# Performance work log

Measured on AMD Instinct MI355X. Metric: run time of the kernel, lower is better.

The kernel has to match this reference:

```python
import jax, jax.numpy as jnp
import numpy as np

B, NP, NS, CIN, COUT, CMID = 16, 1024, 32, 64, 128, 32

def _bn(x, g, b, m, v, eps=1e-5):
    # inference-mode BatchNorm over channel axis 1
    sh = (1, -1) + (1,) * (x.ndim - 2)
    return (x - m.reshape(sh)) * (g.reshape(sh) * jax.lax.rsqrt(v.reshape(sh) + eps)) + b.reshape(sh)

def setup_inputs() -> dict:
    key = jax.random.key(0)
    ks = jax.random.split(key, 10)
    f = jax.random.normal
    return {
        "new_xyz": f(ks[0], (B, 3, NP), jnp.float32),
        "grouped_xyz": f(ks[1], (B, NP, NS, 3), jnp.float32),
        "grouped_feature": f(ks[2], (B, CIN, NS, NP), jnp.float32),
        "wh_w": f(ks[3], (CMID, 3), jnp.float32) * 0.1,
        "wh_b": f(ks[4], (CMID,), jnp.float32) * 0.1,
        "wh_g": jnp.ones((CMID,), jnp.float32), "wh_beta": jnp.zeros((CMID,), jnp.float32),
        "wh_m": jnp.zeros((CMID,), jnp.float32), "wh_v": jnp.ones((CMID,), jnp.float32),
        "n1_w": f(ks[5], (16, 1), jnp.float32) * 0.1,
        "n1_b": f(ks[6], (16,), jnp.float32) * 0.1,
        "n1_g": jnp.ones((16,), jnp.float32), "n1_beta": jnp.zeros((16,), jnp.float32),
        "n1_m": jnp.zeros((16,), jnp.float32), "n1_v": jnp.ones((16,), jnp.float32),
        "n2_w": f(ks[7], (1, 16), jnp.float32) * 0.1,
        "n2_b": f(ks[8], (1,), jnp.float32) * 0.1,
        "n2_g": jnp.ones((1,), jnp.float32), "n2_beta": jnp.zeros((1,), jnp.float32),
        "n2_m": jnp.zeros((1,), jnp.float32), "n2_v": jnp.ones((1,), jnp.float32),
        "out_w": f(ks[9], (COUT, CIN, CMID), jnp.float32) * 0.05,
        "out_b": jnp.zeros((COUT,), jnp.float32),
        "out_g": jnp.ones((COUT,), jnp.float32), "out_beta": jnp.zeros((COUT,), jnp.float32),
        "out_m": jnp.zeros((COUT,), jnp.float32), "out_v": jnp.ones((COUT,), jnp.float32),
    }

def reference(new_xyz, grouped_xyz, grouped_feature,
              wh_w, wh_b, wh_g, wh_beta, wh_m, wh_v,
              n1_w, n1_b, n1_g, n1_beta, n1_m, n1_v,
              n2_w, n2_b, n2_g, n2_beta, n2_m, n2_v,
              out_w, out_b, out_g, out_beta, out_m, out_v):
    # kernel_density_estimation_ball mutates in place: after i=0 the reference
    # point is zero, so ONLY sample 0 is actually zeroed. Replicate exactly.
    gx = grouped_xyz.at[:, :, 0, :].set(0.0)          # [B,NP,NS,3]
    density = jnp.sum(gx, axis=-1, keepdims=True)      # [B,NP,NS,1]
    density = jnp.where(density < 1e-10, 1e-10, density)
    inv = 1.0 / density
    ds = inv / jnp.max(inv, axis=2, keepdims=True)     # [B,NP,NS,1]
    # weight net on the mutated grouped_xyz
    gx_p = jnp.transpose(gx, (0, 3, 1, 2))             # [B,3,NP,NS]
    w = jax.nn.relu(_bn(jnp.einsum('bcps,oc->bops', gx_p, wh_w) + wh_b.reshape(1, -1, 1, 1),
                        wh_g, wh_beta, wh_m, wh_v))    # [B,CMID,NP,NS]
    # nonlinear density transform
    dsp = jnp.transpose(ds, (0, 3, 1, 2))              # [B,1,NP,NS]
    d1 = jax.nn.relu(_bn(jnp.einsum('bcps,oc->bops', dsp, n1_w) + n1_b.reshape(1, -1, 1, 1),
                         n1_g, n1_beta, n1_m, n1_v))   # [B,16,NP,NS]
    d2 = jax.nn.sigmoid(_bn(jnp.einsum('bcps,oc->bops', d1, n2_w) + n2_b.reshape(1, -1, 1, 1),
                            n2_g, n2_beta, n2_m, n2_v))  # [B,1,NP,NS]
    # density-scaled features, then batched matmul with positional weights
    gf = jnp.transpose(grouped_feature, (0, 1, 3, 2)) * d2      # [B,CIN,NP,NS]
    mm = jnp.einsum('bcps,bmps->bcpm', gf, w)                   # [B,CIN,NP,CMID]
    # out_conv: Conv2d(CIN->COUT, kernel (1,CMID)) collapses last dim
    out = jnp.einsum('bcpk,ock->bop', mm, out_w) + out_b.reshape(1, -1, 1)  # [B,COUT,NP]
    out = _bn(out, out_g, out_beta, out_m, out_v)
    return (jnp.transpose(new_xyz, (0, 2, 1)), out)
```

## Files before the change

### kernel.cpp

```cpp
#include <hip/hip_runtime.h>
#include <hip/hip_bf16.h>


#define NPP 1024
#define NSS 32

typedef __attribute__((ext_vector_type(8))) short short8;
typedef __attribute__((ext_vector_type(4))) float f32x4;

__device__ __forceinline__ unsigned short f2bf(float x) {
  union { float f; unsigned u; } v; v.f = x;
  unsigned r = v.u + 0x7FFFu + ((v.u >> 16) & 1u);
  return (unsigned short)(r >> 16);
}

__device__ __forceinline__ unsigned long long pack4bf(f32x4 v) {
  return (unsigned long long)f2bf(v[0])
       | ((unsigned long long)f2bf(v[1]) << 16)
       | ((unsigned long long)f2bf(v[2]) << 32)
       | ((unsigned long long)f2bf(v[3]) << 48);
}

__global__ __launch_bounds__(256) void k_prep(
    const float* __restrict__ out_w, const float* __restrict__ new_xyz,
    unsigned short* __restrict__ owc, float* __restrict__ out0)
{
  int bid = blockIdx.x, t = threadIdx.x;
  if (bid < 128) {
    int gid = bid * 256 + t;
    int lane = gid & 63, ci = gid >> 6;
    int hi = ci & 1, tt = (ci >> 1) & 15, cblk = (ci >> 5) & 3, w = ci >> 7;
    int sg = lane >> 4, l15 = lane & 15;
    int o = w*32 + hi*16 + l15;
    int k = tt*2 + (sg >> 1);
    int cbase = cblk*16 + (sg & 1)*8;
    short8 vv;
    #pragma unroll
    for (int j = 0; j < 8; ++j)
      vv[j] = (short)f2bf(out_w[(o*64 + cbase + j)*32 + k]);
    *(short8*)&owc[(size_t)gid * 8] = vv;
  } else {
    int idx = (bid - 128) * 256 + t;
    int b = idx / 3072, r = idx - b*3072, p = r / 3, d = r - p*3;
    out0[idx] = new_xyz[(b*3 + d)*NPP + p];
  }
}

__global__ __launch_bounds__(256) void k_xpose(
    const float* __restrict__ F, unsigned short* __restrict__ Fb)
{
  int bid = blockIdx.x;
  int xcd = bid & 7, idx = bid >> 3;
  int b = xcd * 2 + (idx >> 4), ptq = idx & 15;
  int t = threadIdx.x;
  int sg = t >> 6, l15 = (t >> 2) & 15, k4 = t & 3;

  #pragma unroll
  for (int cblk = 0; cblk < 4; ++cblk) {
    int c = cblk * 16 + l15;
    const float* src = &F[((size_t)((b*64 + c)*32) + sg*8)*NPP + ptq*64 + k4*4];
    #pragma unroll
    for (int ptl = 0; ptl < 4; ++ptl) {
      float4 v[8];
      #pragma unroll
      for (int j = 0; j < 8; ++j) v[j] = *(const float4*)&src[(size_t)j*NPP + ptl*16];
      unsigned short* tb = &Fb[(size_t)(b*64 + ptq*4 + ptl)*32768 + cblk*512 + sg*128 + l15*8];
      #pragma unroll
      for (int pwl = 0; pwl < 4; ++pwl) {
        unsigned o0 = (unsigned)f2bf(((const float*)&v[0])[pwl]) | ((unsigned)f2bf(((const float*)&v[1])[pwl]) << 16);
        unsigned o1 = (unsigned)f2bf(((const float*)&v[2])[pwl]) | ((unsigned)f2bf(((const float*)&v[3])[pwl]) << 16);
        unsigned o2 = (unsigned)f2bf(((const float*)&v[4])[pwl]) | ((unsigned)f2bf(((const float*)&v[5])[pwl]) << 16);
        unsigned o3 = (unsigned)f2bf(((const float*)&v[6])[pwl]) | ((unsigned)f2bf(((const float*)&v[7])[pwl]) << 16);
        uint4 wv = {o0, o1, o2, o3};
        *(uint4*)&tb[(size_t)(k4*4 + pwl)*2048] = wv;
      }
    }
  }
}

struct Smem2 {
  float gxd[64*32*4];
  unsigned short wd[16*32*32];
  char mm[64*1024];
  float cst[192];
};

__global__ __launch_bounds__(512, 1) void k_main(
    const unsigned short* __restrict__ Fb, const float* __restrict__ GX,
    const float* __restrict__ whw, const float* __restrict__ whb,
    const float* __restrict__ whg, const float* __restrict__ whbeta,
    const float* __restrict__ whm, const float* __restrict__ whv,
    const float* __restrict__ n1w, const float* __restrict__ n1b,
    const float* __restrict__ n1g, const float* __restrict__ n1beta,
    const float* __restrict__ n1m, const float* __restrict__ n1v,
    const float* __restrict__ n2w, const float* __restrict__ n2b,
    const float* __restrict__ n2g, const float* __restrict__ n2beta,
    const float* __restrict__ n2m, const float* __restrict__ n2v,
    const unsigned short* __restrict__ OWc,
    const float* __restrict__ ob, const float* __restrict__ og,
    const float* __restrict__ obeta, const float* __restrict__ om,
    const float* __restrict__ ov,
    float* __restrict__ out1)
{
  __shared__ Smem2 sm;
  int xcd = blockIdx.x & 7, idx = blockIdx.x >> 3;
  int b = xcd*2 + (idx >> 4), pt64 = idx & 15;
  int p0 = pt64 * 64;
  int t = threadIdx.x, w = t >> 6, lane = t & 63;
  int l15 = lane & 15, sg = lane >> 4;

  int pp8 = t >> 3, si8 = t & 7;
  const float* g = &GX[(size_t)(b*NPP + p0 + pp8)*96 + si8*12];
  float4 f0 = *(const float4*)g;
  float4 f1 = *(const float4*)(g + 4);
  float4 f2 = *(const float4*)(g + 8);

  if (t < 32) {
    float sc = whg[t] * rsqrtf(whv[t] + 1e-5f);
    sm.cst[t]    = whw[t*3+0] * sc;
    sm.cst[32+t] = whw[t*3+1] * sc;
    sm.cst[64+t] = whw[t*3+2] * sc;
    sm.cst[96+t] = (whb[t] - whm[t]) * sc + whbeta[t];
  } else if (t < 48) {
    int i = t - 32;
    float sc = n1g[i] * rsqrtf(n1v[i] + 1e-5f);
    sm.cst[128+i] = n1w[i] * sc;
    sm.cst[144+i] = (n1b[i] - n1m[i]) * sc + n1beta[i];
  } else if (t < 64) {
    int i = t - 48;
    float sc = n2g[0] * rsqrtf(n2v[0] + 1e-5f);
    sm.cst[160+i] = n2w[i] * sc;
    if (i == 0) sm.cst[176] = (n2b[0] - n2m[0]) * sc + n2beta[0];
  }
  __syncthreads();

  {
    float xs[4], ys[4], zs[4], inv[4];
    xs[0]=f0.x; ys[0]=f0.y; zs[0]=f0.z;
    xs[1]=f0.w; ys[1]=f1.x; zs[1]=f1.y;
    xs[2]=f1.z; ys[2]=f1.w; zs[2]=f2.x;
    xs[3]=f2.y; ys[3]=f2.z; zs[3]=f2.w;
    if (si8 == 0) { xs[0]=0.f; ys[0]=0.f; zs[0]=0.f; }
    float mx = 0.f;
    #pragma unroll
    for (int u = 0; u < 4; ++u) {
      float den = xs[u] + ys[u] + zs[u];
      if (den < 1e-10f) den = 1e-10f;
      inv[u] = 1.0f / den;
      mx = fmaxf(mx, inv[u]);
    }
    #pragma unroll
    for (int m = 1; m < 8; m <<= 1) mx = fmaxf(mx, __shfl_xor(mx, m, 8));
    #pragma unroll
    for (int u = 0; u < 4; ++u) {
      float ds = inv[u] / mx;
      float acc = sm.cst[176];
      #pragma unroll
      for (int i = 0; i < 16; ++i) {
        float d1 = fmaxf(ds * sm.cst[128+i] + sm.cst[144+i], 0.f);
        acc += d1 * sm.cst[160+i];
      }
      float d2 = 1.0f / (1.0f + expf(-acc));
      float4 st = {xs[u], ys[u], zs[u], d2};
      *(float4*)&sm.gxd[(size_t)(pp8*32 + si8*4 + u)*4] = st;
    }
  }
  __syncthreads();

  const f32x4 z4 = {0,0,0,0};
  int phKh = (lane >> 4) & 1;
  int phPp = w*2 + (lane >> 5);
  int phSi = lane & 15;
  int ppA = w*2, ppB = w*2 + 1;
  int c0 = l15*32 + sg*8;

  short8 afA[4][4], afB[4][4];
  short8 bfrA[4][2], bfrB[4][2];
  #pragma unroll
  for (int pg = 0; pg < 4; ++pg) {
    const unsigned short* ft = &Fb[(size_t)(b*64 + pt64*4 + pg)*32768 + sg*128 + l15*8];
    #pragma unroll
    for (int cblk = 0; cblk < 4; ++cblk) {
      afA[pg][cblk] = *(const short8*)&ft[(size_t)ppA*2048 + cblk*512];
      afB[pg][cblk] = *(const short8*)&ft[(size_t)ppB*2048 + cblk*512];
    }
    const float4 ga = *(const float4*)&sm.gxd[(size_t)((pg*16 + phPp)*32 + phSi*2)*4];
    const float4 gb = *(const float4*)&sm.gxd[(size_t)((pg*16 + phPp)*32 + phSi*2 + 1)*4];
    #pragma unroll
    for (int ki = 0; ki < 16; ++ki) {
      int k = phKh*16 + ki;
      float a0 = sm.cst[k], a1 = sm.cst[32+k], a2 = sm.cst[64+k], bc = sm.cst[96+k];
      float w0 = fmaxf(ga.x*a0 + ga.y*a1 + ga.z*a2 + bc, 0.f) * ga.w;
      float w1 = fmaxf(gb.x*a0 + gb.y*a1 + gb.z*a2 + bc, 0.f) * gb.w;
      unsigned r = (unsigned)f2bf(w0) | ((unsigned)f2bf(w1) << 16);
      *(unsigned*)&sm.wd[(phPp*32 + k)*32 + phSi*2] = r;
    }
    #pragma unroll
    for (int kh = 0; kh < 2; ++kh) {
      bfrA[pg][kh] = *(const short8*)&sm.wd[(ppA*32 + kh*16 + l15)*32 + sg*8];
      bfrB[pg][kh] = *(const short8*)&sm.wd[(ppB*32 + kh*16 + l15)*32 + sg*8];
    }
  }

  int w4 = w & 3, gp0 = (w >> 2) * 2;
  f32x4 acc00 = {0,0,0,0}, acc10 = {0,0,0,0}, acc01 = {0,0,0,0}, acc11 = {0,0,0,0};
  int rowG0 = gp0*16 + l15, rowG1 = (gp0+1)*16 + l15;
  unsigned sw0 = (rowG0 & 15) << 4, sw1 = (rowG1 & 15) << 4;
  const char* bbase0 = sm.mm + rowG0*1024;
  const char* bbase1 = sm.mm + rowG1*1024;

  #pragma unroll
  for (int cblk = 0; cblk < 4; ++cblk) {
    #pragma unroll
    for (int pg = 0; pg < 4; ++pg) {
      f32x4 mA0 = __builtin_amdgcn_mfma_f32_16x16x32_bf16(afA[pg][cblk], bfrA[pg][0], z4, 0,0,0);
      f32x4 mA1 = __builtin_amdgcn_mfma_f32_16x16x32_bf16(afA[pg][cblk], bfrA[pg][1], z4, 0,0,0);
      f32x4 mB0 = __builtin_amdgcn_mfma_f32_16x16x32_bf16(afB[pg][cblk], bfrB[pg][0], z4, 0,0,0);
      f32x4 mB1 = __builtin_amdgcn_mfma_f32_16x16x32_bf16(afB[pg][cblk], bfrB[pg][1], z4, 0,0,0);
      int rowA = pg*16 + ppA, rowB = pg*16 + ppB;
      unsigned swA = (rowA & 15) << 4, swB = (rowB & 15) << 4;
      char* bA = sm.mm + rowA*1024;
      char* bB = sm.mm + rowB*1024;
      *(unsigned long long*)(bA + ((c0      ) ^ swA)) = pack4bf(mA0);
      *(unsigned long long*)(bA + ((c0 + 512) ^ swA)) = pack4bf(mA1);
      *(unsigned long long*)(bB + ((c0      ) ^ swB)) = pack4bf(mB0);
      *(unsigned long long*)(bB + ((c0 + 512) ^ swB)) = pack4bf(mB1);
    }
    __syncthreads();
    {
      const unsigned short* ac = &OWc[(size_t)((w4*4 + cblk)*16)*1024 + lane*8];
      #pragma unroll 8
      for (int tt = 0; tt < 16; ++tt) {
        short8 a0 = *(const short8*)&ac[tt*1024];
        short8 a1 = *(const short8*)&ac[tt*1024 + 512];
        int col = sg*16 + tt*64;
        short8 b0 = *(const short8*)(bbase0 + (col ^ sw0));
        short8 b1 = *(const short8*)(bbase1 + (col ^ sw1));
        acc00 = __builtin_amdgcn_mfma_f32_16x16x32_bf16(a0, b0, acc00, 0,0,0);
        acc10 = __builtin_amdgcn_mfma_f32_16x16x32_bf16(a1, b0, acc10, 0,0,0);
        acc01 = __builtin_amdgcn_mfma_f32_16x16x32_bf16(a0, b1, acc01, 0,0,0);
        acc11 = __builtin_amdgcn_mfma_f32_16x16x32_bf16(a1, b1, acc11, 0,0,0);
      }
    }
    __syncthreads();
  }

  #pragma unroll
  for (int hi = 0; hi < 2; ++hi)
    #pragma unroll
    for (int gg = 0; gg < 2; ++gg) {
      f32x4 a = hi ? (gg ? acc11 : acc10) : (gg ? acc01 : acc00);
      #pragma unroll
      for (int r = 0; r < 4; ++r) {
        int o = w4*32 + hi*16 + sg*4 + r;
        float sc = og[o] * rsqrtf(ov[o] + 1e-5f);
        float dd = (ob[o] - om[o]) * sc + obeta[o];
        out1[(size_t)(b*128 + o)*NPP + p0 + (gp0+gg)*16 + l15] = a[r] * sc + dd;
      }
    }
}

extern "C" void kernel_launch(void* const* d_in, const int* in_sizes, int n_in,
                              void* d_out, int out_size, void* d_ws, size_t ws_size,
                              hipStream_t stream) {
  (void)in_sizes; (void)n_in; (void)out_size; (void)ws_size;
  const float* new_xyz = (const float*)d_in[0];
  const float* gxyz    = (const float*)d_in[1];
  const float* gfeat   = (const float*)d_in[2];
  const float* whw     = (const float*)d_in[3];
  const float* whb     = (const float*)d_in[4];
  const float* whg     = (const float*)d_in[5];
  const float* whbeta  = (const float*)d_in[6];
  const float* whm     = (const float*)d_in[7];
  const float* whv     = (const float*)d_in[8];
  const float* n1w     = (const float*)d_in[9];
  const float* n1b     = (const float*)d_in[10];
  const float* n1g     = (const float*)d_in[11];
  const float* n1beta  = (const float*)d_in[12];
  const float* n1m     = (const float*)d_in[13];
  const float* n1v     = (const float*)d_in[14];
  const float* n2w     = (const float*)d_in[15];
  const float* n2b     = (const float*)d_in[16];
  const float* n2g     = (const float*)d_in[17];
  const float* n2beta  = (const float*)d_in[18];
  const float* n2m     = (const float*)d_in[19];
  const float* n2v     = (const float*)d_in[20];
  const float* out_w   = (const float*)d_in[21];
  const float* out_b   = (const float*)d_in[22];
  const float* out_g   = (const float*)d_in[23];
  const float* out_bt  = (const float*)d_in[24];
  const float* out_m   = (const float*)d_in[25];
  const float* out_v   = (const float*)d_in[26];

  unsigned short* owc = (unsigned short*)d_ws;
  unsigned short* fb  = owc + (1u << 18);
  float* out0 = (float*)d_out;
  float* out1 = out0 + 16*1024*3;

  hipLaunchKernelGGL(k_prep,  dim3(320), dim3(256), 0, stream, out_w, new_xyz, owc, out0);
  hipLaunchKernelGGL(k_xpose, dim3(256), dim3(256), 0, stream, gfeat, fb);
  hipLaunchKernelGGL(k_main,  dim3(256), dim3(512), 0, stream,
      fb, gxyz, whw, whb, whg, whbeta, whm, whv,
      n1w, n1b, n1g, n1beta, n1m, n1v,
      n2w, n2b, n2g, n2beta, n2m, n2v,
      owc, out_b, out_g, out_bt, out_m, out_v, out1);
}
```

Baseline: 87.02 us.

## Fuse feature transpose into main kernel with LDS staging and prefetch

Removes the separate k_xpose kernel, which converted grouped_feature to bf16 in a transposed layout in global memory. k_main now loads fp32 features directly, converts them and writes them into a swizzled LDS buffer that is unioned with the phase-0 scratch. It prefetches the next channel block's features into registers while the current block's MFMAs run. This saves a kernel launch and a full bf16 write and read round trip through global memory, at the cost of extra syncthreads, LDS traffic and register pressure in k_main.

```diff
diff --git a/kernel.cpp b/kernel.cpp
--- a/kernel.cpp
+++ b/kernel.cpp
@@ -3,7 +3,6 @@
 
 
 #define NPP 1024
-#define NSS 32
 
 typedef __attribute__((ext_vector_type(8))) short short8;
 typedef __attribute__((ext_vector_type(4))) float f32x4;
@@ -46,47 +45,20 @@
   }
 }
 
-__global__ __launch_bounds__(256) void k_xpose(
-    const float* __restrict__ F, unsigned short* __restrict__ Fb)
-{
-  int bid = blockIdx.x;
-  int xcd = bid & 7, idx = bid >> 3;
-  int b = xcd * 2 + (idx >> 4), ptq = idx & 15;
-  int t = threadIdx.x;
-  int sg = t >> 6, l15 = (t >> 2) & 15, k4 = t & 3;
-
-  #pragma unroll
-  for (int cblk = 0; cblk < 4; ++cblk) {
-    int c = cblk * 16 + l15;
-    const float* src = &F[((size_t)((b*64 + c)*32) + sg*8)*NPP + ptq*64 + k4*4];
-    #pragma unroll
-    for (int ptl = 0; ptl < 4; ++ptl) {
-      float4 v[8];
-      #pragma unroll
-      for (int j = 0; j < 8; ++j) v[j] = *(const float4*)&src[(size_t)j*NPP + ptl*16];
-      unsigned short* tb = &Fb[(size_t)(b*64 + ptq*4 + ptl)*32768 + cblk*512 + sg*128 + l15*8];
-      #pragma unroll
-      for (int pwl = 0; pwl < 4; ++pwl) {
-        unsigned o0 = (unsigned)f2bf(((const float*)&v[0])[pwl]) | ((unsigned)f2bf(((const float*)&v[1])[pwl]) << 16);
-        unsigned o1 = (unsigned)f2bf(((const float*)&v[2])[pwl]) | ((unsigned)f2bf(((const float*)&v[3])[pwl]) << 16);
-        unsigned o2 = (unsigned)f2bf(((const float*)&v[4])[pwl]) | ((unsigned)f2bf(((const float*)&v[5])[pwl]) << 16);
-        unsigned o3 = (unsigned)f2bf(((const float*)&v[6])[pwl]) | ((unsigned)f2bf(((const float*)&v[7])[pwl]) << 16);
-        uint4 wv = {o0, o1, o2, o3};
-        *(uint4*)&tb[(size_t)(k4*4 + pwl)*2048] = wv;
-      }
-    }
-  }
-}
-
-struct Smem2 {
-  float gxd[64*32*4];
-  unsigned short wd[16*32*32];
+struct Smem3 {
+  union {
+    struct {
+      float gxd[64*32*4];
+      unsigned short wd[16*32*32];
+    } ph0;
+    unsigned short fs[32768];
+  } u;
   char mm[64*1024];
   float cst[192];
 };
 
 __global__ __launch_bounds__(512, 1) void k_main(
-    const unsigned short* __restrict__ Fb, const float* __restrict__ GX,
+    const float* __restrict__ F, const float* __restrict__ GX,
     const float* __restrict__ whw, const float* __restrict__ whb,
     const float* __restrict__ whg, const float* __restrict__ whbeta,
     const float* __restrict__ whm, const float* __restrict__ whv,
@@ -102,12 +74,24 @@
     const float* __restrict__ ov,
     float* __restrict__ out1)
 {
-  __shared__ Smem2 sm;
+  __shared__ Smem3 sm;
   int xcd = blockIdx.x & 7, idx = blockIdx.x >> 3;
   int b = xcd*2 + (idx >> 4), pt64 = idx & 15;
   int p0 = pt64 * 64;
   int t = threadIdx.x, w = t >> 6, lane = t & 63;
   int l15 = lane & 15, sg = lane >> 4;
+
+  int so = w & 3, ch = w >> 2;
+  int q4 = lane & 3, c3 = (lane >> 2) & 7, jh = (lane >> 5) & 1;
+  int c_l = ch*8 + c3, s0 = so*8 + jh*4;
+  const float* fsrc0 = &F[((size_t)((b*64 + c_l)*32) + s0)*NPP + p0 + q4*4];
+
+  float4 fv[4][4];
+  #pragma unroll
+  for (int jj = 0; jj < 4; ++jj)
+    #pragma unroll
+    for (int qg = 0; qg < 4; ++qg)
+      fv[jj][qg] = *(const float4*)&fsrc0[(size_t)jj*NPP + qg*16];
 
   int pp8 = t >> 3, si8 = t & 7;
   const float* g = &GX[(size_t)(b*NPP + p0 + pp8)*96 + si8*12];
@@ -162,7 +146,7 @@
       }
       float d2 = 1.0f / (1.0f + expf(-acc));
       float4 st = {xs[u], ys[u], zs[u], d2};
-      *(float4*)&sm.gxd[(size_t)(pp8*32 + si8*4 + u)*4] = st;
+      *(float4*)&sm.u.ph0.gxd[(size_t)(pp8*32 + si8*4 + u)*4] = st;
     }
   }
   __syncthreads();
@@ -174,18 +158,11 @@
   int ppA = w*2, ppB = w*2 + 1;
   int c0 = l15*32 + sg*8;
 
-  short8 afA[4][4], afB[4][4];
   short8 bfrA[4][2], bfrB[4][2];
   #pragma unroll
   for (int pg = 0; pg < 4; ++pg) {
-    const unsigned short* ft = &Fb[(size_t)(b*64 + pt64*4 + pg)*32768 + sg*128 + l15*8];
-    #pragma unroll
-    for (int cblk = 0; cblk < 4; ++cblk) {
-      afA[pg][cblk] = *(const short8*)&ft[(size_t)ppA*2048 + cblk*512];
-      afB[pg][cblk] = *(const short8*)&ft[(size_t)ppB*2048 + cblk*512];
-    }
-    const float4 ga = *(const float4*)&sm.gxd[(size_t)((pg*16 + phPp)*32 + phSi*2)*4];
-    const float4 gb = *(const float4*)&sm.gxd[(size_t)((pg*16 + phPp)*32 + phSi*2 + 1)*4];
+    const float4 ga = *(const float4*)&sm.u.ph0.gxd[(size_t)((pg*16 + phPp)*32 + phSi*2)*4];
+    const float4 gb = *(const float4*)&sm.u.ph0.gxd[(size_t)((pg*16 + phPp)*32 + phSi*2 + 1)*4];
     #pragma unroll
     for (int ki = 0; ki < 16; ++ki) {
       int k = phKh*16 + ki;
@@ -193,14 +170,15 @@
       float w0 = fmaxf(ga.x*a0 + ga.y*a1 + ga.z*a2 + bc, 0.f) * ga.w;
       float w1 = fmaxf(gb.x*a0 + gb.y*a1 + gb.z*a2 + bc, 0.f) * gb.w;
       unsigned r = (unsigned)f2bf(w0) | ((unsigned)f2bf(w1) << 16);
-      *(unsigned*)&sm.wd[(phPp*32 + k)*32 + phSi*2] = r;
+      *(unsigned*)&sm.u.ph0.wd[(phPp*32 + k)*32 + phSi*2] = r;
     }
     #pragma unroll
     for (int kh = 0; kh < 2; ++kh) {
-      bfrA[pg][kh] = *(const short8*)&sm.wd[(ppA*32 + kh*16 + l15)*32 + sg*8];
-      bfrB[pg][kh] = *(const short8*)&sm.wd[(ppB*32 + kh*16 + l15)*32 + sg*8];
-    }
-  }
+      bfrA[pg][kh] = *(const short8*)&sm.u.ph0.wd[(ppA*32 + kh*16 + l15)*32 + sg*8];
+      bfrB[pg][kh] = *(const short8*)&sm.u.ph0.wd[(ppB*32 + kh*16 + l15)*32 + sg*8];
+    }
+  }
+  __syncthreads();
 
   int w4 = w & 3, gp0 = (w >> 2) * 2;
   f32x4 acc00 = {0,0,0,0}, acc10 = {0,0,0,0}, acc01 = {0,0,0,0}, acc11 = {0,0,0,0};
@@ -208,23 +186,57 @@
   unsigned sw0 = (rowG0 & 15) << 4, sw1 = (rowG1 & 15) << 4;
   const char* bbase0 = sm.mm + rowG0*1024;
   const char* bbase1 = sm.mm + rowG1*1024;
+  int fsbase = so*128 + c_l*8 + jh*4;
 
   #pragma unroll
   for (int cblk = 0; cblk < 4; ++cblk) {
     #pragma unroll
+    for (int qg = 0; qg < 4; ++qg)
+      #pragma unroll
+      for (int pi = 0; pi < 4; ++pi) {
+        int p = qg*16 + q4*4 + pi;
+        unsigned sw = (unsigned)(p & 15) << 3;
+        #pragma unroll
+        for (int jp = 0; jp < 2; ++jp) {
+          unsigned u = (unsigned)f2bf(((const float*)&fv[jp*2][qg])[pi])
+                     | ((unsigned)f2bf(((const float*)&fv[jp*2+1][qg])[pi]) << 16);
+          unsigned fidx = (unsigned)(p*512 + fsbase + jp*2) ^ sw;
+          *(unsigned*)&sm.u.fs[fidx] = u;
+        }
+      }
+    __syncthreads();
+
+    short8 afA[4], afB[4];
+    unsigned swA = (unsigned)(ppA & 15) << 3, swB = (unsigned)(ppB & 15) << 3;
+    #pragma unroll
     for (int pg = 0; pg < 4; ++pg) {
-      f32x4 mA0 = __builtin_amdgcn_mfma_f32_16x16x32_bf16(afA[pg][cblk], bfrA[pg][0], z4, 0,0,0);
-      f32x4 mA1 = __builtin_amdgcn_mfma_f32_16x16x32_bf16(afA[pg][cblk], bfrA[pg][1], z4, 0,0,0);
-      f32x4 mB0 = __builtin_amdgcn_mfma_f32_16x16x32_bf16(afB[pg][cblk], bfrB[pg][0], z4, 0,0,0);
-      f32x4 mB1 = __builtin_amdgcn_mfma_f32_16x16x32_bf16(afB[pg][cblk], bfrB[pg][1], z4, 0,0,0);
+      unsigned iA = (unsigned)((pg*16 + ppA)*512 + sg*128 + l15*8) ^ swA;
+      unsigned iB = (unsigned)((pg*16 + ppB)*512 + sg*128 + l15*8) ^ swB;
+      afA[pg] = *(const short8*)&sm.u.fs[iA];
+      afB[pg] = *(const short8*)&sm.u.fs[iB];
+    }
+    if (cblk < 3) {
+      const float* fsrc = fsrc0 + (size_t)(cblk + 1) * 16 * 32 * NPP;
+      #pragma unroll
+      for (int jj = 0; jj < 4; ++jj)
+        #pragma unroll
+        for (int qg = 0; qg < 4; ++qg)
+          fv[jj][qg] = *(const float4*)&fsrc[(size_t)jj*NPP + qg*16];
+    }
+    #pragma unroll
+    for (int pg = 0; pg < 4; ++pg) {
+      f32x4 mA0 = __builtin_amdgcn_mfma_f32_16x16x32_bf16(afA[pg], bfrA[pg][0], z4, 0,0,0);
+      f32x4 mA1 = __builtin_amdgcn_mfma_f32_16x16x32_bf16(afA[pg], bfrA[pg][1], z4, 0,0,0);
+      f32x4 mB0 = __builtin_amdgcn_mfma_f32_16x16x32_bf16(afB[pg], bfrB[pg][0], z4, 0,0,0);
+      f32x4 mB1 = __builtin_amdgcn_mfma_f32_16x16x32_bf16(afB[pg], bfrB[pg][1], z4, 0,0,0);
       int rowA = pg*16 + ppA, rowB = pg*16 + ppB;
-      unsigned swA = (rowA & 15) << 4, swB = (rowB & 15) << 4;
+      unsigned swa = (rowA & 15) << 4, swb = (rowB & 15) << 4;
       char* bA = sm.mm + rowA*1024;
       char* bB = sm.mm + rowB*1024;
-      *(unsigned long long*)(bA + ((c0      ) ^ swA)) = pack4bf(mA0);
-      *(unsigned long long*)(bA + ((c0 + 512) ^ swA)) = pack4bf(mA1);
-      *(unsigned long long*)(bB + ((c0      ) ^ swB)) = pack4bf(mB0);
-      *(unsigned long long*)(bB + ((c0 + 512) ^ swB)) = pack4bf(mB1);
+      *(unsigned long long*)(bA + ((c0      ) ^ swa)) = pack4bf(mA0);
+      *(unsigned long long*)(bA + ((c0 + 512) ^ swa)) = pack4bf(mA1);
+      *(unsigned long long*)(bB + ((c0      ) ^ swb)) = pack4bf(mB0);
+      *(unsigned long long*)(bB + ((c0 + 512) ^ swb)) = pack4bf(mB1);
     }
     __syncthreads();
     {
@@ -293,14 +305,12 @@
   const float* out_v   = (const float*)d_in[26];
 
   unsigned short* owc = (unsigned short*)d_ws;
-  unsigned short* fb  = owc + (1u << 18);
   float* out0 = (float*)d_out;
   float* out1 = out0 + 16*1024*3;
 
-  hipLaunchKernelGGL(k_prep,  dim3(320), dim3(256), 0, stream, out_w, new_xyz, owc, out0);
-  hipLaunchKernelGGL(k_xpose, dim3(256), dim3(256), 0, stream, gfeat, fb);
-  hipLaunchKernelGGL(k_main,  dim3(256), dim3(512), 0, stream,
-      fb, gxyz, whw, whb, whg, whbeta, whm, whv,
+  hipLaunchKernelGGL(k_prep, dim3(320), dim3(256), 0, stream, out_w, new_xyz, owc, out0);
+  hipLaunchKernelGGL(k_main, dim3(256), dim3(512), 0, stream,
+      gfeat, gxyz, whw, whb, whg, whbeta, whm, whv,
       n1w, n1b, n1g, n1beta, n1m, n1v,
       n2w, n2b, n2g, n2beta, n2m, n2v,
       owc, out_b, out_g, out_bt, out_m, out_v, out1);
```

New measurement: 70.97 us (median of 2 runs). 1.23x faster.
